# Optimization experiments

Hardware: AMD Instinct MI355X
Metric: run time of the kernel (lower is better)

The kernel has to match this reference:

```python
import jax, jax.numpy as jnp
import numpy as np

H = 2048  # config.hidden_num


def setup_inputs() -> dict:
    key = jax.random.key(0)
    ks = jax.random.split(key, 19)
    def rn(k, shape, s=0.05):
        return jax.random.normal(k, shape, dtype=jnp.float32) * s
    return {
        # forward args
        "xt": rn(ks[0], (7,), 1.0),
        "h0": rn(ks[1], (1, 34), 1.0),
        "feature_t": rn(ks[2], (1, 462), 1.0),
        "number": rn(ks[3], (1,), 1.0),
        "restrict": rn(ks[4], (1,), 1.0),
        # 7 distinct GRUCells, stacked on a leading axis for lax.scan
        "w_ih": rn(ks[5], (7, 3 * H, 1)),
        "w_hh": rn(ks[6], (7, 3 * H, H)),
        "b_ih": rn(ks[7], (7, 3 * H)),
        "b_hh": rn(ks[8], (7, 3 * H)),
        # embedding: Linear(34, H)
        "emb_w": rn(ks[9], (H, 34)),
        "emb_b": rn(ks[10], (H,)),
        # feature MLP: 462 -> 66 -> 66 -> H
        "f1_w": rn(ks[11], (66, 462)),
        "f1_b": rn(ks[12], (66,)),
        "f2_w": rn(ks[13], (66, 66)),
        "f2_b": rn(ks[14], (66,)),
        "f3_w": rn(ks[15], (H, 66)),
        "f3_b": rn(ks[16], (H,)),
        # out_linear: Linear(H + 2, 1)
        "out_w": rn(ks[17], (1, H + 2)),
        "out_b": rn(ks[18], (1,)),
    }


def reference(xt, h0, feature_t, number, restrict,
              w_ih, w_hh, b_ih, b_hh,
              emb_w, emb_b,
              f1_w, f1_b, f2_w, f2_b, f3_w, f3_b,
              out_w, out_b):
    # feature MLP (note: no nonlinearities in the original)
    feat = feature_t.reshape(feature_t.shape[0], -1)           # (1, 462)
    fd = feat @ f1_w.T + f1_b                                  # (1, 66)
    fd = fd @ f2_w.T + f2_b                                    # (1, 66)
    fd = fd @ f3_w.T + f3_b                                    # (1, H)
    hid = h0 @ emb_w.T + emb_b + fd                            # (1, H)

    def gru_step(h, xs):
        x, wi, wh, bi, bh = xs
        gi = x.reshape(1, 1) @ wi.T + bi                       # (1, 3H)
        gh = h @ wh.T + bh                                     # (1, 3H)
        i_r, i_z, i_n = jnp.split(gi, 3, axis=1)
        h_r, h_z, h_n = jnp.split(gh, 3, axis=1)
        r = jax.nn.sigmoid(i_r + h_r)
        z = jax.nn.sigmoid(i_z + h_z)
        n = jnp.tanh(i_n + r * h_n)
        h_new = (1.0 - z) * n + z * h                          # (1, H)
        return h_new, None

    h7, _ = jax.lax.scan(gru_step, hid, (xt, w_ih, w_hh, b_ih, b_hh))
    hid_out = jnp.concatenate([h7, restrict.reshape(1, 1), number.reshape(1, 1)], axis=1)
    return hid_out @ out_w.T + out_b                           # (1, 1)
```

## Files before the change

### kernel.cpp

```cpp
#include <hip/hip_runtime.h>
#include <hip/hip_bf16.h>

#define HDIM 2048

__global__ __launch_bounds__(128) void mlp_kernel(
    const float* __restrict__ feat,
    const float* __restrict__ f1_w,
    const float* __restrict__ f1_b,
    const float* __restrict__ f2_w,
    const float* __restrict__ f2_b,
    float* __restrict__ fd2_out)
{
    __shared__ float fd1[66];
    const int t = threadIdx.x;
    if (t < 66) {
        float s = f1_b[t];
        const float* row = f1_w + t * 462;
        for (int k = 0; k < 462; ++k) s = fmaf(row[k], feat[k], s);
        fd1[t] = s;
    }
    __syncthreads();
    if (t < 66) {
        float s = f2_b[t];
        const float* row = f2_w + t * 66;
        for (int k = 0; k < 66; ++k) s = fmaf(row[k], fd1[k], s);
        fd2_out[t] = s;
    }
}

__global__ __launch_bounds__(256) void hid_kernel(
    const float* __restrict__ h0,
    const float* __restrict__ emb_w,
    const float* __restrict__ emb_b,
    const float* __restrict__ f3_w,
    const float* __restrict__ f3_b,
    const float* __restrict__ fd2,
    float* __restrict__ h_out)
{
    const int j = blockIdx.x * blockDim.x + threadIdx.x;
    if (j >= HDIM) return;
    float s = emb_b[j] + f3_b[j];
    const float* er = emb_w + j * 34;
    for (int k = 0; k < 34; ++k) s = fmaf(er[k], h0[k], s);
    const float* fr = f3_w + j * 66;
    for (int k = 0; k < 66; ++k) s = fmaf(fr[k], fd2[k], s);
    h_out[j] = s;
}

__global__ __launch_bounds__(256) void gru_step_kernel(
    const float* __restrict__ w_hh,
    const float* __restrict__ w_ih,
    const float* __restrict__ b_ih,
    const float* __restrict__ b_hh,
    const float* __restrict__ xt,
    const int step,
    const float* __restrict__ h_in,
    float* __restrict__ h_out)
{
    const int wave = (blockIdx.x * blockDim.x + threadIdx.x) >> 6;
    const int lane = threadIdx.x & 63;
    const int j = wave;

    const float4* hv4 = (const float4*)h_in;
    const float4* wr  = (const float4*)(w_hh + (size_t)j * HDIM);
    const float4* wz  = (const float4*)(w_hh + (size_t)(HDIM + j) * HDIM);
    const float4* wn  = (const float4*)(w_hh + (size_t)(2 * HDIM + j) * HDIM);

    float sr = 0.f, sz = 0.f, sn = 0.f;
#pragma unroll
    for (int i = 0; i < 8; ++i) {
        const int idx = i * 64 + lane;
        const float4 h4 = hv4[idx];
        const float4 a  = wr[idx];
        const float4 b  = wz[idx];
        const float4 c  = wn[idx];
        sr = fmaf(a.x, h4.x, fmaf(a.y, h4.y, fmaf(a.z, h4.z, fmaf(a.w, h4.w, sr))));
        sz = fmaf(b.x, h4.x, fmaf(b.y, h4.y, fmaf(b.z, h4.z, fmaf(b.w, h4.w, sz))));
        sn = fmaf(c.x, h4.x, fmaf(c.y, h4.y, fmaf(c.z, h4.z, fmaf(c.w, h4.w, sn))));
    }
#pragma unroll
    for (int off = 32; off > 0; off >>= 1) {
        sr += __shfl_down(sr, off);
        sz += __shfl_down(sz, off);
        sn += __shfl_down(sn, off);
    }

    if (lane == 0) {
        const float x = xt[step];
        const float gir = fmaf(x, w_ih[j],            b_ih[j]);
        const float giz = fmaf(x, w_ih[HDIM + j],     b_ih[HDIM + j]);
        const float gin = fmaf(x, w_ih[2 * HDIM + j], b_ih[2 * HDIM + j]);
        const float ghr = sr + b_hh[j];
        const float ghz = sz + b_hh[HDIM + j];
        const float ghn = sn + b_hh[2 * HDIM + j];
        const float r = 1.f / (1.f + expf(-(gir + ghr)));
        const float z = 1.f / (1.f + expf(-(giz + ghz)));
        const float n = tanhf(fmaf(r, ghn, gin));
        h_out[j] = fmaf(z, h_in[j] - n, n);
    }
}

__global__ __launch_bounds__(256) void out_kernel(
    const float* __restrict__ h7,
    const float* __restrict__ out_w,
    const float* __restrict__ out_b,
    const float* __restrict__ restr,
    const float* __restrict__ number,
    float* __restrict__ out)
{
    __shared__ float red[256];
    const int t = threadIdx.x;
    float s = 0.f;
    for (int k = t; k < HDIM; k += 256) s = fmaf(out_w[k], h7[k], s);
    red[t] = s;
    __syncthreads();
#pragma unroll
    for (int off = 128; off > 0; off >>= 1) {
        if (t < off) red[t] += red[t + off];
        __syncthreads();
    }
    if (t == 0) {
        out[0] = red[0] + restr[0] * out_w[HDIM] + number[0] * out_w[HDIM + 1]
               + out_b[0];
    }
}

extern "C" void kernel_launch(void* const* d_in, const int* in_sizes, int n_in,
                              void* d_out, int out_size, void* d_ws, size_t ws_size,
                              hipStream_t stream) {
    const float* xt     = (const float*)d_in[0];
    const float* h0     = (const float*)d_in[1];
    const float* feat   = (const float*)d_in[2];
    const float* number = (const float*)d_in[3];
    const float* restr  = (const float*)d_in[4];
    const float* w_ih   = (const float*)d_in[5];
    const float* w_hh   = (const float*)d_in[6];
    const float* b_ih   = (const float*)d_in[7];
    const float* b_hh   = (const float*)d_in[8];
    const float* emb_w  = (const float*)d_in[9];
    const float* emb_b  = (const float*)d_in[10];
    const float* f1_w   = (const float*)d_in[11];
    const float* f1_b   = (const float*)d_in[12];
    const float* f2_w   = (const float*)d_in[13];
    const float* f2_b   = (const float*)d_in[14];
    const float* f3_w   = (const float*)d_in[15];
    const float* f3_b   = (const float*)d_in[16];
    const float* out_w  = (const float*)d_in[17];
    const float* out_b  = (const float*)d_in[18];

    float* ws    = (float*)d_ws;
    float* fd2   = ws;
    float* hbuf0 = ws + 256;
    float* hbuf1 = ws + 256 + HDIM;

    mlp_kernel<<<1, 128, 0, stream>>>(feat, f1_w, f1_b, f2_w, f2_b, fd2);
    hid_kernel<<<HDIM / 256, 256, 0, stream>>>(h0, emb_w, emb_b, f3_w, f3_b, fd2,
                                               hbuf0);

    float* bufs[2] = {hbuf0, hbuf1};
    for (int s = 0; s < 7; ++s) {
        const float* hin = bufs[s & 1];
        float* hout      = bufs[(s + 1) & 1];
        gru_step_kernel<<<(HDIM * 64) / 256, 256, 0, stream>>>(
            w_hh + (size_t)s * 3 * HDIM * HDIM,
            w_ih + (size_t)s * 3 * HDIM,
            b_ih + (size_t)s * 3 * HDIM,
            b_hh + (size_t)s * 3 * HDIM,
            xt, s, hin, hout);
    }

    out_kernel<<<1, 256, 0, stream>>>(bufs[7 & 1], out_w, out_b, restr, number,
                                      (float*)d_out);
}
```

Measured before the change: 118.9 us.

## Split GRU rows across two waves and parallelize MLP and hidden init

The GRU step kernel now assigns each hidden row to two waves that each reduce half of the 2048-long dot products, then combines the partials through shared memory, doubling the grid to 1024 blocks. The first MLP layer switches from one thread per output row to one wave per row with a shuffle reduction, which removes a long serial 462-element loop. The hidden-init kernel stages h0 and fd2 in shared memory and uses float2 weight loads. The GRU change adds a block barrier and shared-memory traffic in exchange for more memory parallelism on a bandwidth-bound matvec.

```diff
diff --git a/kernel.cpp b/kernel.cpp
--- a/kernel.cpp
+++ b/kernel.cpp
@@ -3,7 +3,7 @@
 
 #define HDIM 2048
 
-__global__ __launch_bounds__(128) void mlp_kernel(
+__global__ __launch_bounds__(512) void mlp_kernel(
     const float* __restrict__ feat,
     const float* __restrict__ f1_w,
     const float* __restrict__ f1_b,
@@ -12,14 +12,19 @@
     float* __restrict__ fd2_out)
 {
     __shared__ float fd1[66];
-    const int t = threadIdx.x;
-    if (t < 66) {
-        float s = f1_b[t];
-        const float* row = f1_w + t * 462;
-        for (int k = 0; k < 462; ++k) s = fmaf(row[k], feat[k], s);
-        fd1[t] = s;
-    }
-    __syncthreads();
+    const int wid  = threadIdx.x >> 6;
+    const int lane = threadIdx.x & 63;
+
+    for (int o = wid; o < 66; o += 8) {
+        const float* row = f1_w + o * 462;
+        float s = 0.f;
+        for (int k = lane; k < 462; k += 64) s = fmaf(row[k], feat[k], s);
+#pragma unroll
+        for (int off = 32; off > 0; off >>= 1) s += __shfl_down(s, off);
+        if (lane == 0) fd1[o] = s + f1_b[o];
+    }
+    __syncthreads();
+    const int t = threadIdx.x;
     if (t < 66) {
         float s = f2_b[t];
         const float* row = f2_w + t * 66;
@@ -37,13 +42,28 @@
     const float* __restrict__ fd2,
     float* __restrict__ h_out)
 {
-    const int j = blockIdx.x * blockDim.x + threadIdx.x;
+    __shared__ float s_h0[34];
+    __shared__ float s_fd2[66];
+    const int t = threadIdx.x;
+    if (t < 34) s_h0[t] = h0[t];
+    if (t < 66) s_fd2[t] = fd2[t];
+    __syncthreads();
+
+    const int j = blockIdx.x * blockDim.x + t;
     if (j >= HDIM) return;
     float s = emb_b[j] + f3_b[j];
-    const float* er = emb_w + j * 34;
-    for (int k = 0; k < 34; ++k) s = fmaf(er[k], h0[k], s);
-    const float* fr = f3_w + j * 66;
-    for (int k = 0; k < 66; ++k) s = fmaf(fr[k], fd2[k], s);
+    const float2* er = (const float2*)(emb_w + j * 34);
+#pragma unroll
+    for (int k = 0; k < 17; ++k) {
+        const float2 w = er[k];
+        s = fmaf(w.x, s_h0[2 * k], fmaf(w.y, s_h0[2 * k + 1], s));
+    }
+    const float2* fr = (const float2*)(f3_w + j * 66);
+#pragma unroll
+    for (int k = 0; k < 33; ++k) {
+        const float2 w = fr[k];
+        s = fmaf(w.x, s_fd2[2 * k], fmaf(w.y, s_fd2[2 * k + 1], s));
+    }
     h_out[j] = s;
 }
 
@@ -57,18 +77,22 @@
     const float* __restrict__ h_in,
     float* __restrict__ h_out)
 {
-    const int wave = (blockIdx.x * blockDim.x + threadIdx.x) >> 6;
+    __shared__ float part[4][3];
+
+    const int wid  = threadIdx.x >> 6;
     const int lane = threadIdx.x & 63;
-    const int j = wave;
-
-    const float4* hv4 = (const float4*)h_in;
-    const float4* wr  = (const float4*)(w_hh + (size_t)j * HDIM);
-    const float4* wz  = (const float4*)(w_hh + (size_t)(HDIM + j) * HDIM);
-    const float4* wn  = (const float4*)(w_hh + (size_t)(2 * HDIM + j) * HDIM);
+    const int row  = blockIdx.x * 2 + (wid >> 1);
+    const int half = wid & 1;
+
+    const int base4 = half * 256;
+    const float4* hv4 = (const float4*)h_in + base4;
+    const float4* wr  = (const float4*)(w_hh + (size_t)row * HDIM) + base4;
+    const float4* wz  = (const float4*)(w_hh + (size_t)(HDIM + row) * HDIM) + base4;
+    const float4* wn  = (const float4*)(w_hh + (size_t)(2 * HDIM + row) * HDIM) + base4;
 
     float sr = 0.f, sz = 0.f, sn = 0.f;
 #pragma unroll
-    for (int i = 0; i < 8; ++i) {
+    for (int i = 0; i < 4; ++i) {
         const int idx = i * 64 + lane;
         const float4 h4 = hv4[idx];
         const float4 a  = wr[idx];
@@ -84,15 +108,26 @@
         sz += __shfl_down(sz, off);
         sn += __shfl_down(sn, off);
     }
-
     if (lane == 0) {
+        part[wid][0] = sr;
+        part[wid][1] = sz;
+        part[wid][2] = sn;
+    }
+    __syncthreads();
+
+    const int t = threadIdx.x;
+    if (t < 2) {
+        const int j = blockIdx.x * 2 + t;
+        const float psr = part[2 * t][0] + part[2 * t + 1][0];
+        const float psz = part[2 * t][1] + part[2 * t + 1][1];
+        const float psn = part[2 * t][2] + part[2 * t + 1][2];
         const float x = xt[step];
         const float gir = fmaf(x, w_ih[j],            b_ih[j]);
         const float giz = fmaf(x, w_ih[HDIM + j],     b_ih[HDIM + j]);
         const float gin = fmaf(x, w_ih[2 * HDIM + j], b_ih[2 * HDIM + j]);
-        const float ghr = sr + b_hh[j];
-        const float ghz = sz + b_hh[HDIM + j];
-        const float ghn = sn + b_hh[2 * HDIM + j];
+        const float ghr = psr + b_hh[j];
+        const float ghz = psz + b_hh[HDIM + j];
+        const float ghn = psn + b_hh[2 * HDIM + j];
         const float r = 1.f / (1.f + expf(-(gir + ghr)));
         const float z = 1.f / (1.f + expf(-(giz + ghz)));
         const float n = tanhf(fmaf(r, ghn, gin));
@@ -153,7 +188,7 @@
     float* hbuf0 = ws + 256;
     float* hbuf1 = ws + 256 + HDIM;
 
-    mlp_kernel<<<1, 128, 0, stream>>>(feat, f1_w, f1_b, f2_w, f2_b, fd2);
+    mlp_kernel<<<1, 512, 0, stream>>>(feat, f1_w, f1_b, f2_w, f2_b, fd2);
     hid_kernel<<<HDIM / 256, 256, 0, stream>>>(h0, emb_w, emb_b, f3_w, f3_b, fd2,
                                                hbuf0);
 
@@ -161,7 +196,7 @@
     for (int s = 0; s < 7; ++s) {
         const float* hin = bufs[s & 1];
         float* hout      = bufs[(s + 1) & 1];
-        gru_step_kernel<<<(HDIM * 64) / 256, 256, 0, stream>>>(
+        gru_step_kernel<<<HDIM / 2, 256, 0, stream>>>(
             w_hh + (size_t)s * 3 * HDIM * HDIM,
             w_ih + (size_t)s * 3 * HDIM,
             b_ih + (size_t)s * 3 * HDIM,
```

New measurement: 122.8 us. 1.03x slower.

## Prefetch next GRU step's weights into cache and parallelize MLP/hid kernels

Applied to the files above, without the earlier changes.

Each GRU step kernel now also touches one float per 64-byte line of the next step's w_hh slice, so those lines are pulled into the last-level cache while the current step computes. The hid kernel does the same for step 0's weights, and both it and the first MLP layer are rewritten to use a wave per output row with shuffle reductions instead of a serial per-thread loop. The goal is to hide DRAM latency for the 48MB-per-step weight stream. In exchange it adds memory traffic to every step, and the prefetch only pays off if the lines survive in cache until the next launch.

```diff
diff --git a/kernel.cpp b/kernel.cpp
--- a/kernel.cpp
+++ b/kernel.cpp
@@ -1,9 +1,8 @@
 #include <hip/hip_runtime.h>
-#include <hip/hip_bf16.h>
 
 #define HDIM 2048
 
-__global__ __launch_bounds__(128) void mlp_kernel(
+__global__ __launch_bounds__(256) void mlp_kernel(
     const float* __restrict__ feat,
     const float* __restrict__ f1_w,
     const float* __restrict__ f1_b,
@@ -12,14 +11,18 @@
     float* __restrict__ fd2_out)
 {
     __shared__ float fd1[66];
+    const int wid  = threadIdx.x >> 6;
+    const int lane = threadIdx.x & 63;
+    for (int o = wid; o < 66; o += 4) {
+        const float* row = f1_w + o * 462;
+        float s = 0.f;
+        for (int k = lane; k < 462; k += 64) s = fmaf(row[k], feat[k], s);
+#pragma unroll
+        for (int off = 32; off; off >>= 1) s += __shfl_down(s, off);
+        if (!lane) fd1[o] = s + f1_b[o];
+    }
+    __syncthreads();
     const int t = threadIdx.x;
-    if (t < 66) {
-        float s = f1_b[t];
-        const float* row = f1_w + t * 462;
-        for (int k = 0; k < 462; ++k) s = fmaf(row[k], feat[k], s);
-        fd1[t] = s;
-    }
-    __syncthreads();
     if (t < 66) {
         float s = f2_b[t];
         const float* row = f2_w + t * 66;
@@ -35,20 +38,36 @@
     const float* __restrict__ f3_w,
     const float* __restrict__ f3_b,
     const float* __restrict__ fd2,
+    const float* __restrict__ w0,
     float* __restrict__ h_out)
 {
-    const int j = blockIdx.x * blockDim.x + threadIdx.x;
-    if (j >= HDIM) return;
-    float s = emb_b[j] + f3_b[j];
-    const float* er = emb_w + j * 34;
-    for (int k = 0; k < 34; ++k) s = fmaf(er[k], h0[k], s);
-    const float* fr = f3_w + j * 66;
-    for (int k = 0; k < 66; ++k) s = fmaf(fr[k], fd2[k], s);
-    h_out[j] = s;
+    const int wid   = threadIdx.x >> 6;
+    const int lane  = threadIdx.x & 63;
+    const int myrow = (blockIdx.x << 2) + wid;
+
+    const int o = lane << 5;
+    const float* n0 = w0 + (size_t)myrow * HDIM;
+    const float* n1 = w0 + (size_t)(HDIM + myrow) * HDIM;
+    const float* n2 = w0 + (size_t)(2 * HDIM + myrow) * HDIM;
+    const float p0 = n0[o], p1 = n0[o + 16];
+    const float p2 = n1[o], p3 = n1[o + 16];
+    const float p4 = n2[o], p5 = n2[o + 16];
+
+    float s = 0.f;
+    if (lane < 34) s = emb_w[myrow * 34 + lane] * h0[lane];
+    s = fmaf(f3_w[myrow * 66 + lane], fd2[lane], s);
+    if (lane < 2) s = fmaf(f3_w[myrow * 66 + 64 + lane], fd2[64 + lane], s);
+#pragma unroll
+    for (int off = 32; off; off >>= 1) s += __shfl_down(s, off);
+    if (!lane) h_out[myrow] = s + emb_b[myrow] + f3_b[myrow];
+
+    asm volatile("" :: "v"(p0), "v"(p1), "v"(p2), "v"(p3), "v"(p4), "v"(p5));
 }
 
 __global__ __launch_bounds__(256) void gru_step_kernel(
     const float* __restrict__ w_hh,
+    const float* __restrict__ w_nx,
+    const int do_pf,
     const float* __restrict__ w_ih,
     const float* __restrict__ b_ih,
     const float* __restrict__ b_hh,
@@ -60,6 +79,17 @@
     const int wave = (blockIdx.x * blockDim.x + threadIdx.x) >> 6;
     const int lane = threadIdx.x & 63;
     const int j = wave;
+
+    float p0 = 0.f, p1 = 0.f, p2 = 0.f, p3 = 0.f, p4 = 0.f, p5 = 0.f;
+    if (do_pf) {
+        const int o = lane << 5;
+        const float* n0 = w_nx + (size_t)j * HDIM;
+        const float* n1 = w_nx + (size_t)(HDIM + j) * HDIM;
+        const float* n2 = w_nx + (size_t)(2 * HDIM + j) * HDIM;
+        p0 = n0[o]; p1 = n0[o + 16];
+        p2 = n1[o]; p3 = n1[o + 16];
+        p4 = n2[o]; p5 = n2[o + 16];
+    }
 
     const float4* hv4 = (const float4*)h_in;
     const float4* wr  = (const float4*)(w_hh + (size_t)j * HDIM);
@@ -79,13 +109,13 @@
         sn = fmaf(c.x, h4.x, fmaf(c.y, h4.y, fmaf(c.z, h4.z, fmaf(c.w, h4.w, sn))));
     }
 #pragma unroll
-    for (int off = 32; off > 0; off >>= 1) {
+    for (int off = 32; off; off >>= 1) {
         sr += __shfl_down(sr, off);
         sz += __shfl_down(sz, off);
         sn += __shfl_down(sn, off);
     }
 
-    if (lane == 0) {
+    if (!lane) {
         const float x = xt[step];
         const float gir = fmaf(x, w_ih[j],            b_ih[j]);
         const float giz = fmaf(x, w_ih[HDIM + j],     b_ih[HDIM + j]);
@@ -98,6 +128,9 @@
         const float n = tanhf(fmaf(r, ghn, gin));
         h_out[j] = fmaf(z, h_in[j] - n, n);
     }
+
+    if (do_pf)
+        asm volatile("" :: "v"(p0), "v"(p1), "v"(p2), "v"(p3), "v"(p4), "v"(p5));
 }
 
 __global__ __launch_bounds__(256) void out_kernel(
@@ -115,11 +148,11 @@
     red[t] = s;
     __syncthreads();
 #pragma unroll
-    for (int off = 128; off > 0; off >>= 1) {
+    for (int off = 128; off; off >>= 1) {
         if (t < off) red[t] += red[t + off];
         __syncthreads();
     }
-    if (t == 0) {
+    if (!t) {
         out[0] = red[0] + restr[0] * out_w[HDIM] + number[0] * out_w[HDIM + 1]
                + out_b[0];
     }
@@ -153,22 +186,23 @@
     float* hbuf0 = ws + 256;
     float* hbuf1 = ws + 256 + HDIM;
 
-    mlp_kernel<<<1, 128, 0, stream>>>(feat, f1_w, f1_b, f2_w, f2_b, fd2);
-    hid_kernel<<<HDIM / 256, 256, 0, stream>>>(h0, emb_w, emb_b, f3_w, f3_b, fd2,
-                                               hbuf0);
+    mlp_kernel<<<1, 256, 0, stream>>>(feat, f1_w, f1_b, f2_w, f2_b, fd2);
+    hid_kernel<<<512, 256, 0, stream>>>(h0, emb_w, emb_b, f3_w, f3_b, fd2,
+                                        w_hh , hbuf0);
 
     float* bufs[2] = {hbuf0, hbuf1};
     for (int s = 0; s < 7; ++s) {
-        const float* hin = bufs[s & 1];
-        float* hout      = bufs[(s + 1) & 1];
+        const int pf = (s < 6) ? 1 : 0;
+        const float* wnx = w_hh + (size_t)(pf ? (s + 1) : s) * 3 * HDIM * HDIM;
         gru_step_kernel<<<(HDIM * 64) / 256, 256, 0, stream>>>(
             w_hh + (size_t)s * 3 * HDIM * HDIM,
+            wnx, pf,
             w_ih + (size_t)s * 3 * HDIM,
             b_ih + (size_t)s * 3 * HDIM,
             b_hh + (size_t)s * 3 * HDIM,
-            xt, s, hin, hout);
-    }
-
-    out_kernel<<<1, 256, 0, stream>>>(bufs[7 & 1], out_w, out_b, restr, number,
+            xt, s, bufs[s & 1], bufs[(s + 1) & 1]);
+    }
+
+    out_kernel<<<1, 256, 0, stream>>>(bufs[1], out_w, out_b, restr, number,
                                       (float*)d_out);
 }
```

Result: slower. 192.0 us (+61.5%).
